# Kernel optimization log

Hardware: AMD Instinct MI355X
Metric: run time of the kernel (lower is better)

## Reference

```python
import jax, jax.numpy as jnp
import numpy as np

R = 4        # p4 rotation group size (n_grid=4)
EPS = 2e-5   # BatchNorm3d eps from the module


def _transform_kernel(w, h):
    # Left action of rotation h on a group-conv kernel [O, I, R, k, k]:
    # cyclic shift along the input-rotation axis + spatial rotation by h*90deg.
    return jnp.rot90(jnp.roll(w, h, axis=2), k=h, axes=(-2, -1))


def _conv2d(x, w, pad):
    return jax.lax.conv_general_dilated(
        x, w, window_strides=(1, 1), padding=[(pad, pad), (pad, pad)],
        dimension_numbers=('NCHW', 'OIHW', 'NCHW'))


def setup_inputs() -> dict:
    key = jax.random.key(0)
    ks = jax.random.split(key, 5)
    B, C, O, H = 16, 96, 48, 66
    E = 2  # C // ratio, ratio = in_channels // 2 = 48
    x = jax.random.normal(ks[0], (B, C, R, H, H), jnp.float32)
    bn_gamma = jnp.ones((C,), jnp.float32)
    bn_beta = jnp.zeros((C,), jnp.float32)
    ca_fc1 = jax.random.normal(ks[1], (E, C, R), jnp.float32) / np.sqrt(C * R)
    ca_fc2 = jax.random.normal(ks[2], (C, E, R), jnp.float32) / np.sqrt(E)
    sa_w = jax.random.normal(ks[3], (1, 2, R, 7, 7), jnp.float32) / np.sqrt(2 * R * 49)
    conv_w = jax.random.normal(ks[4], (O, C, R, 3, 3), jnp.float32) / np.sqrt(C * R * 9)
    return {"x": x, "bn_gamma": bn_gamma, "bn_beta": bn_beta,
            "ca_fc1": ca_fc1, "ca_fc2": ca_fc2, "sa_w": sa_w, "conv_w": conv_w}


def reference(x, bn_gamma, bn_beta, ca_fc1, ca_fc2, sa_w, conv_w):
    B, C, _, H, W = x.shape
    O = conv_w.shape[0]

    # ---- BatchNorm3d (batch statistics over B, R, H, W) + ReLU (pre-activation) ----
    mu = jnp.mean(x, axis=(0, 2, 3, 4), keepdims=True)
    var = jnp.var(x, axis=(0, 2, 3, 4), keepdims=True)
    y = (x - mu) * jax.lax.rsqrt(var + EPS)
    y = y * bn_gamma[None, :, None, None, None] + bn_beta[None, :, None, None, None]
    y = jax.nn.relu(y)

    # ---- fChannelAttentionGG: CBAM-style squeeze-excite per output rotation h ----
    s_avg = jnp.mean(y, axis=(3, 4))  # [B, C, R]
    s_max = jnp.max(y, axis=(3, 4))   # [B, C, R]
    fc1_h = jnp.stack([jnp.roll(ca_fc1, h, axis=2) for h in range(R)])  # [R, E, C, R]
    fc2_h = jnp.stack([jnp.roll(ca_fc2, h, axis=2) for h in range(R)])  # [R, C, E, R]

    def mlp(s):
        hid = jax.nn.relu(jnp.einsum('bcr,hecr->bhe', s, fc1_h))
        return jnp.einsum('bhe,hcer->bhcr', hid, fc2_h)

    ch_att = jax.nn.sigmoid(mlp(s_avg) + mlp(s_max))  # [B, R_out, C, R_in]

    # ---- fSpatialAttentionGG: group conv over channel-pooled [mean, max] maps ----
    u = jnp.concatenate([jnp.mean(y, 1, keepdims=True),
                         jnp.max(y, 1, keepdims=True)], axis=1)  # [B, 2, R, H, W]
    u2 = u.reshape(B, 2 * R, H, W)
    sp = []
    for h in range(R):
        w_h = _transform_kernel(sa_w, h).reshape(1, 2 * R, 7, 7)
        sp.append(_conv2d(u2, w_h, 3)[:, 0])
    sp_att = jax.nn.sigmoid(jnp.stack(sp, axis=1))  # [B, R_out, H, W]

    # ---- attention-gated roto-translation group convolution (fAttConvGG) ----
    outs = []
    for h in range(R):
        yh = y * ch_att[:, h][:, :, :, None, None] * sp_att[:, h][:, None, None, :, :]
        w_h = _transform_kernel(conv_w, h).reshape(O, C * R, 3, 3)
        outs.append(_conv2d(yh.reshape(B, C * R, H, W), w_h, 0))
    out = jnp.stack(outs, axis=2)  # [B, O, R, H-2, W-2]

    # ---- crop + dense concat ----
    return jnp.concatenate([out, x[:, :, :, 1:-1, 1:-1]], axis=1)
```

## Files before the change

### kernel.cpp

```cpp
#include <hip/hip_runtime.h>
#include <hip/hip_bf16.h>
#include <math.h>

constexpr int B_ = 16, C_ = 96, O_ = 48, R_ = 4, H_ = 66, W_ = 66;
constexpr int HW_ = H_ * W_;
constexpr int HO_ = 64, WO_ = 64;
constexpr int OC_ = O_ + C_;
constexpr float EPS_ = 2e-5f;
constexpr int KP_ = 32;
constexpr int NCH_ = (C_*R_)/KP_;
constexpr int PS_ = 36;

constexpr int WS_SUM   = 0;
constexpr int WS_SUMSQ = WS_SUM + C_;
constexpr int WS_SCALE = WS_SUMSQ + C_;
constexpr int WS_SHIFT = WS_SCALE + C_;
constexpr int WS_SAVG  = WS_SHIFT + C_;
constexpr int WS_SMAX  = WS_SAVG + B_*C_*R_;
constexpr int WS_CHATT = WS_SMAX + B_*C_*R_;
constexpr int WS_UMEAN = WS_CHATT + B_*R_*C_*R_;
constexpr int WS_UMAX  = WS_UMEAN + B_*R_*HW_;
constexpr int WS_SPATT = WS_UMAX + B_*R_*HW_;
constexpr int WS_WROT  = WS_SPATT + B_*R_*HW_;

typedef __attribute__((ext_vector_type(8))) __bf16 bf16x8;
typedef __attribute__((ext_vector_type(4))) float f32x4;

__device__ __forceinline__ float sigm(float v){ return 1.0f/(1.0f + __expf(-v)); }

__global__ void k_bn_stats(const float* __restrict__ x, float* __restrict__ ws) {
  int b = blockIdx.x, c = blockIdx.y;
  const float4* p = (const float4*)(x + (size_t)(b*C_ + c) * (R_*HW_));
  int tid = threadIdx.x;
  float s = 0.f, ss = 0.f;
  for (int i = tid; i < R_*HW_/4; i += 256) {
    float4 v = p[i];
    s += v.x + v.y + v.z + v.w;
    ss += v.x*v.x + v.y*v.y + v.z*v.z + v.w*v.w;
  }
  __shared__ float rs[256], rq[256];
  rs[tid] = s; rq[tid] = ss; __syncthreads();
  for (int off = 128; off > 0; off >>= 1) {
    if (tid < off) { rs[tid] += rs[tid+off]; rq[tid] += rq[tid+off]; }
    __syncthreads();
  }
  if (tid == 0) {
    atomicAdd(&ws[WS_SUM + c], rs[0]);
    atomicAdd(&ws[WS_SUMSQ + c], rq[0]);
  }
}

__global__ void k_bn_finalize(const float* __restrict__ gamma, const float* __restrict__ beta,
                              float* __restrict__ ws) {
  int c = threadIdx.x;
  if (c < C_) {
    float n = (float)(B_ * R_ * HW_);
    float mu = ws[WS_SUM + c] / n;
    float var = ws[WS_SUMSQ + c] / n - mu*mu;
    float sc = gamma[c] * rsqrtf(var + EPS_);
    ws[WS_SCALE + c] = sc;
    ws[WS_SHIFT + c] = beta[c] - mu * sc;
  }
}

__global__ void k_sstats(const float* __restrict__ x, float* __restrict__ ws,
                         float* __restrict__ out) {
  int r = blockIdx.x, c = blockIdx.y, b = blockIdx.z;
  int tid = threadIdx.x;
  float sc = ws[WS_SCALE + c], sh = ws[WS_SHIFT + c];
  const float* xp = x + (size_t)((b*C_ + c)*R_ + r) * HW_;
  const float4* p = (const float4*)xp;
  float s = 0.f, m = 0.f;
  for (int i = tid; i < HW_/4; i += 256) {
    float4 v = p[i];
    float a0 = fmaxf(fmaf(v.x, sc, sh), 0.f);
    float a1 = fmaxf(fmaf(v.y, sc, sh), 0.f);
    float a2 = fmaxf(fmaf(v.z, sc, sh), 0.f);
    float a3 = fmaxf(fmaf(v.w, sc, sh), 0.f);
    s += a0+a1+a2+a3; m = fmaxf(fmaxf(fmaxf(m, a0), fmaxf(a1, a2)), a3);
  }
  float* op = out + ((size_t)(b*OC_ + O_ + c)*R_ + r)*((size_t)HO_*WO_);
  for (int e = tid; e < HO_*WO_/4; e += 256) {
    int row = e >> 4, c4 = e & 15;
    const float* sp2 = xp + (row+1)*W_ + c4*4 + 1;
    float4 v = make_float4(sp2[0], sp2[1], sp2[2], sp2[3]);
    *(float4*)(op + row*WO_ + c4*4) = v;
  }
  __shared__ float rs[256], rm[256];
  rs[tid] = s; rm[tid] = m; __syncthreads();
  for (int off = 128; off > 0; off >>= 1) {
    if (tid < off) { rs[tid] += rs[tid+off]; rm[tid] = fmaxf(rm[tid], rm[tid+off]); }
    __syncthreads();
  }
  if (tid == 0) {
    int idx = (b*C_ + c)*R_ + r;
    ws[WS_SAVG + idx] = rs[0] / (float)HW_;
    ws[WS_SMAX + idx] = rm[0];
  }
}

__global__ void k_upool(const float* __restrict__ x, float* __restrict__ ws) {
  int r = blockIdx.y, b = blockIdx.z;
  int pos = blockIdx.x*256 + threadIdx.x;
  if (pos >= HW_) return;
  float s = 0.f, m = 0.f;
  for (int c = 0; c < C_; ++c) {
    float v = fmaxf(fmaf(x[(size_t)((b*C_ + c)*R_ + r)*HW_ + pos],
                         ws[WS_SCALE+c], ws[WS_SHIFT+c]), 0.f);
    s += v; m = fmaxf(m, v);
  }
  int idx = (b*R_ + r)*HW_ + pos;
  ws[WS_UMEAN + idx] = s / (float)C_;
  ws[WS_UMAX + idx] = m;
}

__global__ void k_chatt(const float* __restrict__ fc1, const float* __restrict__ fc2,
                        float* __restrict__ ws) {
  int b = blockIdx.x, tid = threadIdx.x;
  __shared__ float sA[C_*R_], sM[C_*R_], hs[8];
  for (int i = tid; i < C_*R_; i += 256) {
    sA[i] = ws[WS_SAVG + b*C_*R_ + i];
    sM[i] = ws[WS_SMAX + b*C_*R_ + i];
  }
  __syncthreads();
  if (tid < 8) {
    int h = tid >> 1, e = tid & 1;
    float aA = 0.f, aM = 0.f;
    for (int c = 0; c < C_; ++c)
      for (int r = 0; r < R_; ++r) {
        float w = fc1[(e*C_ + c)*R_ + ((r - h) & 3)];
        aA += sA[c*R_ + r] * w;
        aM += sM[c*R_ + r] * w;
      }
    hs[tid] = fmaxf(aA, 0.f) + fmaxf(aM, 0.f);
  }
  __syncthreads();
  for (int idx = tid; idx < R_*C_*R_; idx += 256) {
    int h = idx / (C_*R_);
    int c = (idx % (C_*R_)) / R_;
    int r = idx & 3;
    int rr = (r - h) & 3;
    float v = hs[h*2+0] * fc2[(c*2+0)*R_ + rr]
            + hs[h*2+1] * fc2[(c*2+1)*R_ + rr];
    ws[WS_CHATT + b*R_*C_*R_ + idx] = sigm(v);
  }
}

__global__ void k_spatt(const float* __restrict__ saw, float* __restrict__ ws) {
  int h = blockIdx.y, b = blockIdx.z;
  int tid = threadIdx.x;
  __shared__ float wl[2*R_*49];
  for (int e = tid; e < 2*R_*49; e += 256) {
    int g = e / (R_*49);
    int s = (e / 49) % R_;
    int ij = e % 49;
    int i = ij / 7, j = ij % 7;
    int si, sj;
    if (h == 0)      { si = i;     sj = j;     }
    else if (h == 1) { si = j;     sj = 6 - i; }
    else if (h == 2) { si = 6 - i; sj = 6 - j; }
    else             { si = 6 - j; sj = i;     }
    int srot = (s - h) & 3;
    wl[e] = saw[(g*R_ + srot)*49 + si*7 + sj];
  }
  __syncthreads();
  int pos = blockIdx.x*256 + tid;
  if (pos >= HW_) return;
  int y = pos / W_, xx = pos % W_;
  float acc = 0.f;
  for (int g = 0; g < 2; ++g) {
    const float* u = ws + (g ? WS_UMAX : WS_UMEAN) + (size_t)b*R_*HW_;
    for (int s = 0; s < R_; ++s) {
      const float* up = u + s*HW_;
      const float* wp = wl + (g*R_ + s)*49;
      for (int i = 0; i < 7; ++i) {
        int yy = y + i - 3;
        if (yy < 0 || yy >= H_) continue;
        for (int j = 0; j < 7; ++j) {
          int xc = xx + j - 3;
          if (xc < 0 || xc >= W_) continue;
          acc += up[yy*W_ + xc] * wp[i*7 + j];
        }
      }
    }
  }
  ws[WS_SPATT + (b*R_ + h)*HW_ + pos] = sigm(acc);
}

__global__ void k_wrot(const float* __restrict__ cw, float* __restrict__ ws) {
  int chunk = blockIdx.x, h = blockIdx.y;
  __bf16* wp = (__bf16*)(ws + WS_WROT) + (size_t)(h*NCH_ + chunk)*(O_*9*PS_);
  for (int e = threadIdx.x; e < O_*9*KP_; e += 256) {
    int o = e / (9*KP_);
    int s = e % (9*KP_);
    int tap = s / KP_, pl = s % KP_;
    int p = chunk*KP_ + pl;
    int c = p >> 2, r = p & 3;
    int rr = (r - h) & 3;
    int i = tap / 3, j = tap % 3;
    int si, sj;
    if (h == 0)      { si = i;     sj = j;     }
    else if (h == 1) { si = j;     sj = 2 - i; }
    else if (h == 2) { si = 2 - i; sj = 2 - j; }
    else             { si = 2 - j; sj = i;     }
    wp[(o*9 + tap)*PS_ + pl] = (__bf16)cw[((size_t)(o*C_ + c)*R_ + rr)*9 + si*3 + sj];
  }
}

__global__ __launch_bounds__(512) void k_conv(
    const float* __restrict__ x, const float* __restrict__ ws,
    float* __restrict__ out) {
  int ytile = blockIdx.x, h = blockIdx.y, b = blockIdx.z;
  int y0 = ytile * 4;
  int tid = threadIdx.x;
  int lane = tid & 63, wave = tid >> 6;
  int m = lane & 15, quad = lane >> 4;
  int dy = wave >> 1, gp = (wave & 1) * 2;

  __shared__ __align__(16) __bf16 zl[6*W_*PS_];
  __shared__ __align__(16) __bf16 wl[O_*9*PS_];
  __shared__ float satt_l[6*W_];
  __shared__ float catt_l[C_*R_];
  __shared__ float scl[C_], shl[C_];

  const float* sp = ws + WS_SPATT + (size_t)(b*R_ + h)*HW_;
  for (int e = tid; e < 6*W_; e += 512) satt_l[e] = sp[(y0 + e/W_)*W_ + e%W_];
  const float* chatt = ws + WS_CHATT + (size_t)(b*R_ + h)*C_*R_;
  for (int e = tid; e < C_*R_; e += 512) catt_l[e] = chatt[e];
  for (int e = tid; e < C_; e += 512) { scl[e] = ws[WS_SCALE+e]; shl[e] = ws[WS_SHIFT+e]; }

  f32x4 acc[3][2];
  #pragma unroll
  for (int nt = 0; nt < 3; ++nt)
    #pragma unroll
    for (int gi = 0; gi < 2; ++gi) acc[nt][gi] = (f32x4){0.f,0.f,0.f,0.f};

  const __bf16* wrot = (const __bf16*)(ws + WS_WROT);

  for (int chunk = 0; chunk < NCH_; ++chunk) {
    __syncthreads();
    for (int e = tid; e < KP_*6*33; e += 512) {
      int pl = e / 198;
      int s = e - pl*198;
      int row = s / 33;
      int cp = s - row*33;
      int p = chunk*KP_ + pl;
      int c = p >> 2, r = p & 3;
      const float* xp = x + (size_t)((b*C_ + c)*R_ + r)*HW_ + (y0+row)*W_ + cp*2;
      float2 xv = *(const float2*)xp;
      float sc = scl[c], sh = shl[c];
      float ca = catt_l[p];
      float v0 = fmaxf(fmaf(xv.x, sc, sh), 0.f) * ca * satt_l[row*W_ + cp*2];
      float v1 = fmaxf(fmaf(xv.y, sc, sh), 0.f) * ca * satt_l[row*W_ + cp*2 + 1];
      int zi = (row*W_ + cp*2)*PS_ + pl;
      zl[zi] = (__bf16)v0;
      zl[zi + PS_] = (__bf16)v1;
    }
    {
      const uint4* wsrc = (const uint4*)(wrot + (size_t)(h*NCH_ + chunk)*(O_*9*PS_));
      uint4* wdst = (uint4*)wl;
      for (int e = tid; e < O_*9*PS_/8; e += 512) wdst[e] = wsrc[e];
    }
    __syncthreads();
    #pragma unroll
    for (int i = 0; i < 3; ++i) {
      #pragma unroll
      for (int j = 0; j < 3; ++j) {
        int tap = i*3 + j;
        bf16x8 zf[2], wf[3];
        #pragma unroll
        for (int gi = 0; gi < 2; ++gi) {
          int col = (gp + gi)*16 + m + j;
          zf[gi] = *(const bf16x8*)&zl[((dy + i)*W_ + col)*PS_ + quad*8];
        }
        #pragma unroll
        for (int nt = 0; nt < 3; ++nt)
          wf[nt] = *(const bf16x8*)&wl[((nt*16 + m)*9 + tap)*PS_ + quad*8];
        #pragma unroll
        for (int nt = 0; nt < 3; ++nt)
          #pragma unroll
          for (int gi = 0; gi < 2; ++gi)
            acc[nt][gi] = __builtin_amdgcn_mfma_f32_16x16x32_bf16(
                wf[nt], zf[gi], acc[nt][gi], 0, 0, 0);
      }
    }
  }
  #pragma unroll
  for (int nt = 0; nt < 3; ++nt)
    #pragma unroll
    for (int gi = 0; gi < 2; ++gi) {
      int col = (gp + gi)*16 + m;
      #pragma unroll
      for (int e = 0; e < 4; ++e) {
        int o = nt*16 + quad*4 + e;
        out[((size_t)(b*OC_ + o)*R_ + h)*((size_t)HO_*WO_) + (y0+dy)*WO_ + col] =
            acc[nt][gi][e];
      }
    }
}

extern "C" void kernel_launch(void* const* d_in, const int* in_sizes, int n_in,
                              void* d_out, int out_size, void* d_ws, size_t ws_size,
                              hipStream_t stream) {
  const float* x     = (const float*)d_in[0];
  const float* gamma = (const float*)d_in[1];
  const float* beta  = (const float*)d_in[2];
  const float* fc1   = (const float*)d_in[3];
  const float* fc2   = (const float*)d_in[4];
  const float* saw   = (const float*)d_in[5];
  const float* cw    = (const float*)d_in[6];
  float* out = (float*)d_out;
  float* ws = (float*)d_ws;

  hipMemsetAsync(d_ws, 0, WS_SCALE * sizeof(float), stream);
  k_bn_stats   <<<dim3(B_, C_),                256, 0, stream>>>(x, ws);
  k_bn_finalize<<<1, 128,                           0, stream>>>(gamma, beta, ws);
  k_wrot       <<<dim3(NCH_, R_),              256, 0, stream>>>(cw, ws);
  k_sstats     <<<dim3(R_, C_, B_),            256, 0, stream>>>(x, ws, out);
  k_upool      <<<dim3((HW_+255)/256, R_, B_), 256, 0, stream>>>(x, ws);
  k_chatt      <<<B_, 256,                          0, stream>>>(fc1, fc2, ws);
  k_spatt      <<<dim3((HW_+255)/256, R_, B_), 256, 0, stream>>>(saw, ws);
  k_conv       <<<dim3(16, R_, B_),            512, 0, stream>>>(x, ws, out);
}
```

Measured before the change: 598.5 us.

## Enlarge conv row tile and pre-swizzle weights into MFMA fragment layout

Each conv block now covers 16 output rows instead of 4, so the 2-row halo is staged less often and every weight fragment loaded from LDS feeds 24 MFMAs per wave instead of 6. Weights are pre-permuted into the per-lane MFMA operand order, so each lane reads them with one contiguous 16-byte load. Activations are staged as 8-plane packed vectors. The grid drops to 256 blocks, and each thread holds 24 accumulator tiles, which raises register pressure and may lower occupancy or leave CUs idle.

```diff
diff --git a/kernel.cpp b/kernel.cpp
--- a/kernel.cpp
+++ b/kernel.cpp
@@ -9,7 +9,10 @@
 constexpr float EPS_ = 2e-5f;
 constexpr int KP_ = 32;
 constexpr int NCH_ = (C_*R_)/KP_;
-constexpr int PS_ = 36;
+constexpr int ROWS_ = 16;
+constexpr int SR_ = ROWS_ + 2;
+constexpr int GPC_ = SR_*W_;
+constexpr int WIMG_ = 9*3*64*8;
 
 constexpr int WS_SUM   = 0;
 constexpr int WS_SUMSQ = WS_SUM + C_;
@@ -189,13 +192,15 @@
 
 __global__ void k_wrot(const float* __restrict__ cw, float* __restrict__ ws) {
   int chunk = blockIdx.x, h = blockIdx.y;
-  __bf16* wp = (__bf16*)(ws + WS_WROT) + (size_t)(h*NCH_ + chunk)*(O_*9*PS_);
-  for (int e = threadIdx.x; e < O_*9*KP_; e += 256) {
-    int o = e / (9*KP_);
-    int s = e % (9*KP_);
-    int tap = s / KP_, pl = s % KP_;
-    int p = chunk*KP_ + pl;
-    int c = p >> 2, r = p & 3;
+  __bf16* wp = (__bf16*)(ws + WS_WROT) + (size_t)(h*NCH_ + chunk)*WIMG_;
+  for (int e = threadIdx.x; e < WIMG_; e += 256) {
+    int kk = e & 7;
+    int lane = (e >> 3) & 63;
+    int nt = (e >> 9) % 3;
+    int tap = e / (3*512);
+    int o = nt*16 + (lane & 15);
+    int plane = chunk*KP_ + (lane >> 4)*8 + kk;
+    int c = plane >> 2, r = plane & 3;
     int rr = (r - h) & 3;
     int i = tap / 3, j = tap % 3;
     int si, sj;
@@ -203,100 +208,114 @@
     else if (h == 1) { si = j;     sj = 2 - i; }
     else if (h == 2) { si = 2 - i; sj = 2 - j; }
     else             { si = 2 - j; sj = i;     }
-    wp[(o*9 + tap)*PS_ + pl] = (__bf16)cw[((size_t)(o*C_ + c)*R_ + rr)*9 + si*3 + sj];
-  }
-}
-
-__global__ __launch_bounds__(512) void k_conv(
+    wp[e] = (__bf16)cw[((size_t)(o*C_ + c)*R_ + rr)*9 + si*3 + sj];
+  }
+}
+
+__global__ __launch_bounds__(512, 2) void k_conv(
     const float* __restrict__ x, const float* __restrict__ ws,
     float* __restrict__ out) {
   int ytile = blockIdx.x, h = blockIdx.y, b = blockIdx.z;
-  int y0 = ytile * 4;
+  int y0 = ytile * ROWS_;
   int tid = threadIdx.x;
   int lane = tid & 63, wave = tid >> 6;
   int m = lane & 15, quad = lane >> 4;
-  int dy = wave >> 1, gp = (wave & 1) * 2;
-
-  __shared__ __align__(16) __bf16 zl[6*W_*PS_];
-  __shared__ __align__(16) __bf16 wl[O_*9*PS_];
-  __shared__ float satt_l[6*W_];
+  int colgrp = wave & 1, rowgrp = wave >> 1;
+  int dy0 = rowgrp * 4, colbase = colgrp * 32;
+
+  __shared__ __align__(16) __bf16 zl[4*GPC_*8];
+  __shared__ __align__(16) __bf16 wl[WIMG_];
+  __shared__ float satt_l[GPC_];
   __shared__ float catt_l[C_*R_];
   __shared__ float scl[C_], shl[C_];
 
   const float* sp = ws + WS_SPATT + (size_t)(b*R_ + h)*HW_;
-  for (int e = tid; e < 6*W_; e += 512) satt_l[e] = sp[(y0 + e/W_)*W_ + e%W_];
+  for (int e = tid; e < GPC_; e += 512) satt_l[e] = sp[(y0 + e/W_)*W_ + e%W_];
   const float* chatt = ws + WS_CHATT + (size_t)(b*R_ + h)*C_*R_;
   for (int e = tid; e < C_*R_; e += 512) catt_l[e] = chatt[e];
   for (int e = tid; e < C_; e += 512) { scl[e] = ws[WS_SCALE+e]; shl[e] = ws[WS_SHIFT+e]; }
 
-  f32x4 acc[3][2];
+  f32x4 acc[4][2][3];
   #pragma unroll
-  for (int nt = 0; nt < 3; ++nt)
+  for (int dy = 0; dy < 4; ++dy)
     #pragma unroll
-    for (int gi = 0; gi < 2; ++gi) acc[nt][gi] = (f32x4){0.f,0.f,0.f,0.f};
-
-  const __bf16* wrot = (const __bf16*)(ws + WS_WROT);
+    for (int gi = 0; gi < 2; ++gi)
+      #pragma unroll
+      for (int nt = 0; nt < 3; ++nt) acc[dy][gi][nt] = (f32x4){0.f,0.f,0.f,0.f};
+
+  const __bf16* wglob = (const __bf16*)(ws + WS_WROT) + (size_t)h*NCH_*WIMG_;
+  int sq = tid & 3, sg0 = tid >> 2;
+  __syncthreads();
 
   for (int chunk = 0; chunk < NCH_; ++chunk) {
-    __syncthreads();
-    for (int e = tid; e < KP_*6*33; e += 512) {
-      int pl = e / 198;
-      int s = e - pl*198;
-      int row = s / 33;
-      int cp = s - row*33;
-      int p = chunk*KP_ + pl;
-      int c = p >> 2, r = p & 3;
-      const float* xp = x + (size_t)((b*C_ + c)*R_ + r)*HW_ + (y0+row)*W_ + cp*2;
-      float2 xv = *(const float2*)xp;
-      float sc = scl[c], sh = shl[c];
-      float ca = catt_l[p];
-      float v0 = fmaxf(fmaf(xv.x, sc, sh), 0.f) * ca * satt_l[row*W_ + cp*2];
-      float v1 = fmaxf(fmaf(xv.y, sc, sh), 0.f) * ca * satt_l[row*W_ + cp*2 + 1];
-      int zi = (row*W_ + cp*2)*PS_ + pl;
-      zl[zi] = (__bf16)v0;
-      zl[zi + PS_] = (__bf16)v1;
+    int pbase = chunk*KP_ + sq*8;
+    int cb = pbase >> 2;
+    float sc0 = scl[cb], sh0 = shl[cb], sc1 = scl[cb+1], sh1 = shl[cb+1];
+    float ca[8];
+    #pragma unroll
+    for (int kk = 0; kk < 8; ++kk) ca[kk] = catt_l[pbase + kk];
+
+    for (int g = sg0; g < GPC_; g += 128) {
+      int row = g / W_, col = g - row*W_;
+      const float* xp = x + (size_t)(b*C_*R_ + pbase)*HW_ + (y0+row)*W_ + col;
+      float sa = satt_l[g];
+      bf16x8 pk;
+      #pragma unroll
+      for (int kk = 0; kk < 8; ++kk) {
+        float yv = fmaxf(fmaf(xp[kk*HW_], (kk < 4 ? sc0 : sc1),
+                              (kk < 4 ? sh0 : sh1)), 0.f);
+        pk[kk] = (__bf16)(yv * ca[kk] * sa);
+      }
+      *(bf16x8*)&zl[(sq*GPC_ + g)*8] = pk;
     }
     {
-      const uint4* wsrc = (const uint4*)(wrot + (size_t)(h*NCH_ + chunk)*(O_*9*PS_));
+      const uint4* wsrc = (const uint4*)(wglob + (size_t)chunk*WIMG_);
       uint4* wdst = (uint4*)wl;
-      for (int e = tid; e < O_*9*PS_/8; e += 512) wdst[e] = wsrc[e];
+      for (int e = tid; e < WIMG_/8; e += 512) wdst[e] = wsrc[e];
     }
     __syncthreads();
     #pragma unroll
-    for (int i = 0; i < 3; ++i) {
-      #pragma unroll
-      for (int j = 0; j < 3; ++j) {
+    for (int j = 0; j < 3; ++j) {
+      bf16x8 zf[6][2];
+      #pragma unroll
+      for (int rr = 0; rr < 6; ++rr)
+        #pragma unroll
+        for (int gi = 0; gi < 2; ++gi)
+          zf[rr][gi] = *(const bf16x8*)
+              &zl[(quad*GPC_ + (dy0+rr)*W_ + colbase + gi*16 + m + j)*8];
+      #pragma unroll
+      for (int i = 0; i < 3; ++i) {
         int tap = i*3 + j;
-        bf16x8 zf[2], wf[3];
-        #pragma unroll
-        for (int gi = 0; gi < 2; ++gi) {
-          int col = (gp + gi)*16 + m + j;
-          zf[gi] = *(const bf16x8*)&zl[((dy + i)*W_ + col)*PS_ + quad*8];
-        }
+        bf16x8 wf[3];
         #pragma unroll
         for (int nt = 0; nt < 3; ++nt)
-          wf[nt] = *(const bf16x8*)&wl[((nt*16 + m)*9 + tap)*PS_ + quad*8];
+          wf[nt] = *(const bf16x8*)&wl[((tap*3 + nt)*64 + lane)*8];
         #pragma unroll
-        for (int nt = 0; nt < 3; ++nt)
+        for (int dy = 0; dy < 4; ++dy)
           #pragma unroll
           for (int gi = 0; gi < 2; ++gi)
-            acc[nt][gi] = __builtin_amdgcn_mfma_f32_16x16x32_bf16(
-                wf[nt], zf[gi], acc[nt][gi], 0, 0, 0);
+            #pragma unroll
+            for (int nt = 0; nt < 3; ++nt)
+              acc[dy][gi][nt] = __builtin_amdgcn_mfma_f32_16x16x32_bf16(
+                  wf[nt], zf[dy+i][gi], acc[dy][gi][nt], 0, 0, 0);
       }
     }
+    __syncthreads();
   }
   #pragma unroll
-  for (int nt = 0; nt < 3; ++nt)
+  for (int dy = 0; dy < 4; ++dy)
     #pragma unroll
-    for (int gi = 0; gi < 2; ++gi) {
-      int col = (gp + gi)*16 + m;
-      #pragma unroll
-      for (int e = 0; e < 4; ++e) {
-        int o = nt*16 + quad*4 + e;
-        out[((size_t)(b*OC_ + o)*R_ + h)*((size_t)HO_*WO_) + (y0+dy)*WO_ + col] =
-            acc[nt][gi][e];
-      }
-    }
+    for (int gi = 0; gi < 2; ++gi)
+      #pragma unroll
+      for (int nt = 0; nt < 3; ++nt) {
+        int col = colbase + gi*16 + m;
+        #pragma unroll
+        for (int e = 0; e < 4; ++e) {
+          int o = nt*16 + quad*4 + e;
+          out[((size_t)(b*OC_ + o)*R_ + h)*((size_t)HO_*WO_)
+              + (y0 + dy0 + dy)*WO_ + col] = acc[dy][gi][nt][e];
+        }
+      }
 }
 
 extern "C" void kernel_launch(void* const* d_in, const int* in_sizes, int n_in,
@@ -320,5 +339,5 @@
   k_upool      <<<dim3((HW_+255)/256, R_, B_), 256, 0, stream>>>(x, ws);
   k_chatt      <<<B_, 256,                          0, stream>>>(fc1, fc2, ws);
   k_spatt      <<<dim3((HW_+255)/256, R_, B_), 256, 0, stream>>>(saw, ws);
-  k_conv       <<<dim3(16, R_, B_),            512, 0, stream>>>(x, ws, out);
-}
+  k_conv       <<<dim3(HO_/ROWS_, R_, B_),     512, 0, stream>>>(x, ws, out);
+}
```

Result: faster. 530.5 us (-11.4%).
